# Performance work log

Measured on AMD Instinct MI355X. Metric: run time of the kernel, lower is better.

## Reference

```python
import jax, jax.numpy as jnp
import numpy as np

B, K, H, W = 16, 64, 128, 128


def _centroid(hm):
    # hm: [B, K, H, W] -> rounded soft-argmax keypoints [B, K, 2] (x, y)
    zeta = hm.sum(axis=(2, 3))                                   # [B, K]
    xs = jnp.arange(hm.shape[3], dtype=hm.dtype)                 # j index (width)
    ys = jnp.arange(hm.shape[2], dtype=hm.dtype)                 # i index (height)
    kp_x = jnp.einsum('bkhw,w->bk', hm, xs)                      # Sum j*v
    kp_y = jnp.einsum('bkhw,h->bk', hm, ys)                      # Sum i*v
    return jnp.stack([jnp.round(kp_x / zeta), jnp.round(kp_y / zeta)], axis=-1)


def setup_inputs() -> dict:
    key = jax.random.key(0)
    k1, k2 = jax.random.split(key)
    return {
        'combined_hm_preds': jax.random.uniform(k1, (B, K, H, W), dtype=jnp.float32),
        'tf_combined_hm_preds': jax.random.uniform(k2, (B, K, H, W), dtype=jnp.float32),
        'num_of_kp': K,
    }


def reference(combined_hm_preds, tf_combined_hm_preds, num_of_kp):
    keypoint = _centroid(combined_hm_preds)        # [B, K, 2]
    tf_keypoint = _centroid(tf_combined_hm_preds)  # [B, K, 2]
    return keypoint, tf_keypoint
```

## Files before the change

kernel.cpp:

```cpp
#include <hip/hip_runtime.h>
#include <math.h>


#define HM_H 128
#define HM_W 128

typedef float vf4 __attribute__((ext_vector_type(4)));

__global__ __launch_bounds__(256) void centroid_nt(
    const float* __restrict__ hm0,
    const float* __restrict__ hm1,
    float* __restrict__ out,
    int BK)
{
    const int u  = blockIdx.x;
    const int bk = (u >= BK) ? (u - BK) : u;
    const vf4* __restrict__ p =
        (const vf4*)(((u >= BK) ? hm1 : hm0) + (size_t)bk * (HM_H * HM_W));
    const int t = threadIdx.x;

    const float colb = (float)((t << 2) & (HM_W - 1));
    const float rowb = (float)(t >> 5);

    float s = 0.0f, sx = 0.0f, sy = 0.0f;

#pragma unroll
    for (int m = 0; m < 16; ++m) {
        const vf4 v = __builtin_nontemporal_load(&p[t + m * 256]);
        const float sv = (v[0] + v[1]) + (v[2] + v[3]);
        s  += sv;
        sx += (v[1] + 2.0f * v[2]) + 3.0f * v[3];
        sy += (float)(8 * m) * sv;
    }
    sx += colb * s;
    sy += rowb * s;

    float ss = s;
#pragma unroll
    for (int off = 32; off > 0; off >>= 1) {
        ss += __shfl_down(ss, off, 64);
        sx += __shfl_down(sx, off, 64);
        sy += __shfl_down(sy, off, 64);
    }

    __shared__ float ls[4], lx[4], ly[4];
    const int wid  = t >> 6;
    const int lane = t & 63;
    if (lane == 0) { ls[wid] = ss; lx[wid] = sx; ly[wid] = sy; }
    __syncthreads();

    if (t == 0) {
        const float S = ls[0] + ls[1] + ls[2] + ls[3];
        const float X = lx[0] + lx[1] + lx[2] + lx[3];
        const float Y = ly[0] + ly[1] + ly[2] + ly[3];
        out[u * 2 + 0] = rintf(X / S);
        out[u * 2 + 1] = rintf(Y / S);
    }
}

extern "C" void kernel_launch(void* const* d_in, const int* in_sizes, int n_in,
                              void* d_out, int out_size, void* d_ws, size_t ws_size,
                              hipStream_t stream) {
    const float* hm0 = (const float*)d_in[0];
    const float* hm1 = (const float*)d_in[1];
    float* out = (float*)d_out;

    const int BK     = out_size / 4;
    const int nunits = 2 * BK;

    centroid_nt<<<nunits, 256, 0, stream>>>(hm0, hm1, out, BK);
}
```

Measured before the change: 136.7 us.

## Split each heatmap reduction across two blocks with a finalize kernel

Each heatmap is now reduced by two blocks, each covering half the rows and writing partial sums (S, X, Y) to workspace. A second small kernel combines the partials and computes the rounded centroids. This doubles the grid and halves per-block work, aiming for better occupancy and tail balance across CUs, at the cost of an extra kernel launch and workspace traffic.

```diff
diff --git a/kernel.cpp b/kernel.cpp
--- a/kernel.cpp
+++ b/kernel.cpp
@@ -4,19 +4,23 @@
 
 #define HM_H 128
 #define HM_W 128
+#define PARTS 2
 
 typedef float vf4 __attribute__((ext_vector_type(4)));
 
-__global__ __launch_bounds__(256) void centroid_nt(
+__global__ __launch_bounds__(256) void centroid_nt2(
     const float* __restrict__ hm0,
     const float* __restrict__ hm1,
-    float* __restrict__ out,
+    float* __restrict__ ws,
     int BK)
 {
-    const int u  = blockIdx.x;
-    const int bk = (u >= BK) ? (u - BK) : u;
+    const int gb   = blockIdx.x;
+    const int part = gb & (PARTS - 1);
+    const int u    = gb >> 1;
+    const int bk   = (u >= BK) ? (u - BK) : u;
     const vf4* __restrict__ p =
-        (const vf4*)(((u >= BK) ? hm1 : hm0) + (size_t)bk * (HM_H * HM_W));
+        (const vf4*)(((u >= BK) ? hm1 : hm0) + (size_t)bk * (HM_H * HM_W))
+        + part * (PARTS == 2 ? 2048 : 0);
     const int t = threadIdx.x;
 
     const float colb = (float)((t << 2) & (HM_W - 1));
@@ -25,7 +29,7 @@
     float s = 0.0f, sx = 0.0f, sy = 0.0f;
 
 #pragma unroll
-    for (int m = 0; m < 16; ++m) {
+    for (int m = 0; m < 8; ++m) {
         const vf4 v = __builtin_nontemporal_load(&p[t + m * 256]);
         const float sv = (v[0] + v[1]) + (v[2] + v[3]);
         s  += sv;
@@ -33,12 +37,11 @@
         sy += (float)(8 * m) * sv;
     }
     sx += colb * s;
-    sy += rowb * s;
+    sy += (rowb + (float)(64 * part)) * s;
 
-    float ss = s;
 #pragma unroll
     for (int off = 32; off > 0; off >>= 1) {
-        ss += __shfl_down(ss, off, 64);
+        s  += __shfl_down(s,  off, 64);
         sx += __shfl_down(sx, off, 64);
         sy += __shfl_down(sy, off, 64);
     }
@@ -46,16 +49,33 @@
     __shared__ float ls[4], lx[4], ly[4];
     const int wid  = t >> 6;
     const int lane = t & 63;
-    if (lane == 0) { ls[wid] = ss; lx[wid] = sx; ly[wid] = sy; }
+    if (lane == 0) { ls[wid] = s; lx[wid] = sx; ly[wid] = sy; }
     __syncthreads();
 
     if (t == 0) {
-        const float S = ls[0] + ls[1] + ls[2] + ls[3];
-        const float X = lx[0] + lx[1] + lx[2] + lx[3];
-        const float Y = ly[0] + ly[1] + ly[2] + ly[3];
-        out[u * 2 + 0] = rintf(X / S);
-        out[u * 2 + 1] = rintf(Y / S);
+        ws[gb * 3 + 0] = ls[0] + ls[1] + ls[2] + ls[3];
+        ws[gb * 3 + 1] = lx[0] + lx[1] + lx[2] + lx[3];
+        ws[gb * 3 + 2] = ly[0] + ly[1] + ly[2] + ly[3];
     }
+}
+
+__global__ __launch_bounds__(256) void centroid_nt2_final(
+    const float* __restrict__ ws,
+    float* __restrict__ out,
+    int nunits)
+{
+    const int u = blockIdx.x * 256 + threadIdx.x;
+    if (u >= nunits) return;
+    const float* __restrict__ w = ws + (size_t)u * (PARTS * 3);
+    float S = 0.0f, X = 0.0f, Y = 0.0f;
+#pragma unroll
+    for (int pr = 0; pr < PARTS; ++pr) {
+        S += w[pr * 3 + 0];
+        X += w[pr * 3 + 1];
+        Y += w[pr * 3 + 2];
+    }
+    out[u * 2 + 0] = rintf(X / S);
+    out[u * 2 + 1] = rintf(Y / S);
 }
 
 extern "C" void kernel_launch(void* const* d_in, const int* in_sizes, int n_in,
@@ -64,9 +84,12 @@
     const float* hm0 = (const float*)d_in[0];
     const float* hm1 = (const float*)d_in[1];
     float* out = (float*)d_out;
+    float* ws  = (float*)d_ws;
 
     const int BK     = out_size / 4;
     const int nunits = 2 * BK;
+    const int grid1  = nunits * PARTS;
 
-    centroid_nt<<<nunits, 256, 0, stream>>>(hm0, hm1, out, BK);
+    centroid_nt2<<<grid1, 256, 0, stream>>>(hm0, hm1, ws, BK);
+    centroid_nt2_final<<<(nunits + 255) / 256, 256, 0, stream>>>(ws, out, nunits);
 }
```

After: 138.8 us. Within noise of the previous version (+1.6%).
